# Kernel optimization log

Measured on AMD Instinct MI355X. Metric: run time of the kernel, lower is better.

The kernel has to match this reference:

```python
import jax, jax.numpy as jnp
import numpy as np

B, T, HID, H, DH, K = 2, 1024, 1024, 16, 64, 4
ROPE_BASE = 10000.0
EPS = 1e-6


def _causal_dwconv(x, w, b):
    # x: (B, T, C); w: (C, 1, K) depthwise; causal left-pad K-1, then SiLU
    xc = jnp.transpose(x, (0, 2, 1))  # (B, C, T)
    y = jax.lax.conv_general_dilated(
        xc, w, window_strides=(1,), padding=[(K - 1, 0)],
        dimension_numbers=('NCH', 'OIH', 'NCH'), feature_group_count=xc.shape[1])
    y = y + b[None, :, None]
    return jax.nn.silu(jnp.transpose(y, (0, 2, 1)))


def _rope(x, cos, sin):
    # x: (B, T, H, D); cos/sin: (T, D) with emb = cat(freqs, freqs)
    c = cos[None, :, None, :]
    s = sin[None, :, None, :]
    x1, x2 = x[..., ::2], x[..., 1::2]
    return jnp.concatenate(
        [x1 * c[..., ::2] - x2 * s[..., ::2],
         x1 * s[..., ::2] + x2 * c[..., ::2]], axis=-1)


def _delta_rule(q, k, v, alpha, beta, D_param):
    # q,k,v: (B,T,H,DH); alpha,beta: (B,T,H)
    # S_t = alpha_t * (I - beta_t k_t k_t^T) S_{t-1} + beta_t k_t v_t^T
    # o_t  = q_t^T S_t-1-style readout + D * (q.k) * v   (matches torch einsum 'bhd,bhde->bhe')
    qs = jnp.moveaxis(q, 1, 0).astype(jnp.float32)  # (T,B,H,DH)
    ks = jnp.moveaxis(k, 1, 0).astype(jnp.float32)
    vs = jnp.moveaxis(v, 1, 0).astype(jnp.float32)
    als = jnp.moveaxis(alpha, 1, 0).astype(jnp.float32)  # (T,B,H)
    bes = jnp.moveaxis(beta, 1, 0).astype(jnp.float32)

    def step(S, inp):
        qt, kt, vt, at, bt = inp
        ot = jnp.einsum('bhd,bhde->bhe', qt, S)
        ot = ot + D_param[None, :, None] * jnp.sum(qt * kt, -1, keepdims=True) * vt
        kS = jnp.einsum('bhd,bhde->bhe', kt, S)  # k^T S
        at_ = at[..., None, None]
        bt_ = bt[..., None, None]
        S_new = at_ * (S - bt_ * kt[..., :, None] * kS[..., None, :]) \
                + bt_ * kt[..., :, None] * vt[..., None, :]
        return S_new, ot

    S0 = jnp.zeros((q.shape[0], H, DH, DH), jnp.float32)
    _, outs = jax.lax.scan(step, S0, (qs, ks, vs, als, bes))
    return jnp.moveaxis(outs, 0, 1)  # (B,T,H,DH)


def _forward(x, Wq, Wk, Wv, Wg, Wo, bw, bb, gkw, gkb,
             qcw, qcb, kcw, kcb, vcw, vcb, A_log, D_param, dt_bias, onorm_w):
    Bb, Tt, _ = x.shape
    q = _causal_dwconv(x @ Wq, qcw, qcb).reshape(Bb, Tt, H, DH)
    k = _causal_dwconv(x @ Wk, kcw, kcb).reshape(Bb, Tt, H, DH)
    v = _causal_dwconv(x @ Wv, vcw, vcb).reshape(Bb, Tt, H, DH)

    # RoPE (computed on the fly, fp32)
    t = jnp.arange(Tt, dtype=jnp.float32)
    inv_freq = 1.0 / (ROPE_BASE ** (jnp.arange(0, DH, 2, dtype=jnp.float32) / DH))
    freqs = jnp.outer(t, inv_freq)
    emb = jnp.concatenate([freqs, freqs], -1)
    cos, sin = jnp.cos(emb), jnp.sin(emb)
    q = _rope(q, cos, sin)
    k = _rope(k, cos, sin)

    # L2-normalize q/k (delta-net stability, NOT softmax)
    q = q * jax.lax.rsqrt(jnp.sum(q * q, -1, keepdims=True) + EPS)
    k = k * jax.lax.rsqrt(jnp.sum(k * k, -1, keepdims=True) + EPS)

    beta = jax.nn.sigmoid(x @ bw + bb)  # (B,T,H) writing strength
    alpha = jnp.exp(-jnp.exp(A_log) * jax.nn.softplus(x @ gkw + gkb + dt_bias))  # (B,T,H) decay

    o = _delta_rule(q, k, v, alpha, beta, D_param)  # (B,T,H,DH)

    # gated RMSNorm output: g * silu(RMSNorm(o))
    g = (x @ Wg).reshape(Bb, Tt, H, DH)
    on = o * jax.lax.rsqrt(jnp.mean(o * o, -1, keepdims=True) + EPS) * onorm_w
    o = g * jax.nn.silu(on)
    return o.reshape(Bb, Tt, H * DH) @ Wo


def setup_inputs() -> dict:
    key = jax.random.key(0)
    ks = jax.random.split(key, 20)
    w = lambda i, shape, s=0.02: (jax.random.normal(ks[i], shape, jnp.float32) * s)
    return {
        'x': jax.random.normal(ks[0], (B, T, HID), jnp.float32),
        'Wq': w(1, (HID, H * DH)), 'Wk': w(2, (HID, H * DH)),
        'Wv': w(3, (HID, H * DH)), 'Wg': w(4, (HID, H * DH)),
        'Wo': w(5, (H * DH, HID)),
        'bw': w(6, (HID, H)), 'bb': jnp.zeros((H,), jnp.float32),
        'gkw': w(7, (HID, H)), 'gkb': jnp.zeros((H,), jnp.float32),
        'qcw': w(8, (H * DH, 1, K), 0.3), 'qcb': jnp.zeros((H * DH,), jnp.float32),
        'kcw': w(9, (H * DH, 1, K), 0.3), 'kcb': jnp.zeros((H * DH,), jnp.float32),
        'vcw': w(10, (H * DH, 1, K), 0.3), 'vcb': jnp.zeros((H * DH,), jnp.float32),
        'A_log': jnp.log(jax.random.uniform(ks[11], (H,), jnp.float32, 1.0, 16.0)),
        'D_param': jnp.ones((H,), jnp.float32),
        'dt_bias': jax.random.uniform(ks[12], (H,), jnp.float32, -0.01, 0.01),
        'onorm_w': jnp.ones((DH,), jnp.float32),
    }


def reference(x, Wq, Wk, Wv, Wg, Wo, bw, bb, gkw, gkb,
              qcw, qcb, kcw, kcb, vcw, vcb, A_log, D_param, dt_bias, onorm_w):
    return _forward(x, Wq, Wk, Wv, Wg, Wo, bw, bb, gkw, gkb,
                    qcw, qcb, kcw, kcb, vcw, vcb, A_log, D_param, dt_bias, onorm_w)
```

## Files before the change

kernel.cpp:

```cpp
#include <hip/hip_runtime.h>
#include <hip/hip_bf16.h>
#include <cstdint>

#define T_LEN 1024
#define HIDN  1024
#define NH    16
#define DHD   64

typedef __bf16 bf16x8 __attribute__((ext_vector_type(8)));
typedef float  f32x4  __attribute__((ext_vector_type(4)));

__device__ inline void split8(float4 x0, float4 x1, uint4& hi, uint4& lo) {
  union { __bf16 h[8]; uint4 u; } ph, pl;
  float v[8] = {x0.x, x0.y, x0.z, x0.w, x1.x, x1.y, x1.z, x1.w};
#pragma unroll
  for (int j = 0; j < 8; j++) {
    __bf16 h = (__bf16)v[j];
    ph.h[j] = h;
    pl.h[j] = (__bf16)(v[j] - (float)h);
  }
  hi = ph.u; lo = pl.u;
}

__global__ __launch_bounds__(256) void k_transp_split(
    const float* __restrict__ W0, const float* __restrict__ W1,
    const float* __restrict__ W2, const float* __restrict__ W3,
    const float* __restrict__ W4,
    __bf16* __restrict__ H0, __bf16* __restrict__ H1, __bf16* __restrict__ H2,
    __bf16* __restrict__ H3, __bf16* __restrict__ H4,
    __bf16* __restrict__ L0, __bf16* __restrict__ L1, __bf16* __restrict__ L2,
    __bf16* __restrict__ L3, __bf16* __restrict__ L4) {
  const float* W; __bf16* Th; __bf16* Tl;
  switch (blockIdx.z) {
    case 0: W = W0; Th = H0; Tl = L0; break;
    case 1: W = W1; Th = H1; Tl = L1; break;
    case 2: W = W2; Th = H2; Tl = L2; break;
    case 3: W = W3; Th = H3; Tl = L3; break;
    default: W = W4; Th = H4; Tl = L4; break;
  }
  __shared__ float tile[64][65];
  int tid = threadIdx.x;
  int r0 = tid >> 4;
  int c0 = (tid & 15) * 4;
  int kbase = blockIdx.y * 64, nbase = blockIdx.x * 64;
#pragma unroll
  for (int rr = 0; rr < 4; rr++) {
    int r = r0 + rr * 16;
    float4 v = *(const float4*)(W + (size_t)(kbase + r) * 1024 + nbase + c0);
    tile[r][c0 + 0] = v.x; tile[r][c0 + 1] = v.y;
    tile[r][c0 + 2] = v.z; tile[r][c0 + 3] = v.w;
  }
  __syncthreads();
#pragma unroll
  for (int rr = 0; rr < 4; rr++) {
    int n = r0 + rr * 16;
    union { __bf16 h[4]; unsigned long long u; } ph, pl;
#pragma unroll
    for (int j = 0; j < 4; j++) {
      float v = tile[c0 + j][n];
      __bf16 h = (__bf16)v;
      ph.h[j] = h;
      pl.h[j] = (__bf16)(v - (float)h);
    }
    *(unsigned long long*)(Th + (size_t)(nbase + n) * 1024 + kbase + c0) = ph.u;
    *(unsigned long long*)(Tl + (size_t)(nbase + n) * 1024 + kbase + c0) = pl.u;
  }
}

#define LDT 40
__global__ __launch_bounds__(256) void k_gemm3f(
    const float* __restrict__ Af,
    const __bf16* __restrict__ Bh0, const __bf16* __restrict__ Bh1,
    const __bf16* __restrict__ Bh2, const __bf16* __restrict__ Bh3,
    const __bf16* __restrict__ Bl0, const __bf16* __restrict__ Bl1,
    const __bf16* __restrict__ Bl2, const __bf16* __restrict__ Bl3,
    float* __restrict__ C0, float* __restrict__ C1,
    float* __restrict__ C2, float* __restrict__ C3,
    int Kdim, int Ncols) {
  const __bf16* Bh; const __bf16* Bl; float* C;
  switch (blockIdx.z) {
    case 0: Bh = Bh0; Bl = Bl0; C = C0; break;
    case 1: Bh = Bh1; Bl = Bl1; C = C1; break;
    case 2: Bh = Bh2; Bl = Bl2; C = C2; break;
    default: Bh = Bh3; Bl = Bl3; C = C3; break;
  }
  __shared__ __bf16 Ash[128 * LDT];
  __shared__ __bf16 Asl[128 * LDT];
  __shared__ __bf16 Bsh[128 * LDT];
  __shared__ __bf16 Bsl[128 * LDT];
  const int tid = threadIdx.x;
  const int lane = tid & 63;
  const int wave = tid >> 6;
  const int wr = wave >> 1, wc = wave & 1;
  const int rowA0 = blockIdx.y * 128;
  const int colB0 = blockIdx.x * 128;
  const int sseg = tid & 3;
  const int srow0 = tid >> 2;
  const int srow1 = srow0 + 64;

  f32x4 acc[4][4] = {};

  for (int k0 = 0; k0 < Kdim; k0 += 32) {
    size_t a0 = (size_t)(rowA0 + srow0) * Kdim + k0 + sseg * 8;
    size_t a1 = (size_t)(rowA0 + srow1) * Kdim + k0 + sseg * 8;
    size_t b0 = (size_t)(colB0 + srow0) * Kdim + k0 + sseg * 8;
    size_t b1 = (size_t)(colB0 + srow1) * Kdim + k0 + sseg * 8;
    float4 a00 = *(const float4*)(Af + a0);
    float4 a01 = *(const float4*)(Af + a0 + 4);
    float4 a10 = *(const float4*)(Af + a1);
    float4 a11 = *(const float4*)(Af + a1 + 4);
    uint4 rbh0 = *(const uint4*)(Bh + b0);
    uint4 rbh1 = *(const uint4*)(Bh + b1);
    uint4 rbl0 = *(const uint4*)(Bl + b0);
    uint4 rbl1 = *(const uint4*)(Bl + b1);
    uint4 rah0, ral0, rah1, ral1;
    split8(a00, a01, rah0, ral0);
    split8(a10, a11, rah1, ral1);
    __syncthreads();
    *(uint4*)&Ash[srow0 * LDT + sseg * 8] = rah0;
    *(uint4*)&Ash[srow1 * LDT + sseg * 8] = rah1;
    *(uint4*)&Asl[srow0 * LDT + sseg * 8] = ral0;
    *(uint4*)&Asl[srow1 * LDT + sseg * 8] = ral1;
    *(uint4*)&Bsh[srow0 * LDT + sseg * 8] = rbh0;
    *(uint4*)&Bsh[srow1 * LDT + sseg * 8] = rbh1;
    *(uint4*)&Bsl[srow0 * LDT + sseg * 8] = rbl0;
    *(uint4*)&Bsl[srow1 * LDT + sseg * 8] = rbl1;
    __syncthreads();
    bf16x8 afh[4], afl[4], bfh[4], bfl[4];
#pragma unroll
    for (int mi = 0; mi < 4; mi++) {
      int off = (wr * 64 + mi * 16 + (lane & 15)) * LDT + (lane >> 4) * 8;
      afh[mi] = *(const bf16x8*)&Ash[off];
      afl[mi] = *(const bf16x8*)&Asl[off];
    }
#pragma unroll
    for (int ni = 0; ni < 4; ni++) {
      int off = (wc * 64 + ni * 16 + (lane & 15)) * LDT + (lane >> 4) * 8;
      bfh[ni] = *(const bf16x8*)&Bsh[off];
      bfl[ni] = *(const bf16x8*)&Bsl[off];
    }
#pragma unroll
    for (int mi = 0; mi < 4; mi++)
#pragma unroll
      for (int ni = 0; ni < 4; ni++) {
        acc[mi][ni] = __builtin_amdgcn_mfma_f32_16x16x32_bf16(afh[mi], bfh[ni], acc[mi][ni], 0, 0, 0);
        acc[mi][ni] = __builtin_amdgcn_mfma_f32_16x16x32_bf16(afl[mi], bfh[ni], acc[mi][ni], 0, 0, 0);
        acc[mi][ni] = __builtin_amdgcn_mfma_f32_16x16x32_bf16(afh[mi], bfl[ni], acc[mi][ni], 0, 0, 0);
      }
  }
#pragma unroll
  for (int mi = 0; mi < 4; mi++)
#pragma unroll
    for (int ni = 0; ni < 4; ni++) {
      int col = colB0 + wc * 64 + ni * 16 + (lane & 15);
#pragma unroll
      for (int r = 0; r < 4; r++) {
        int row = rowA0 + wr * 64 + mi * 16 + (lane >> 4) * 4 + r;
        C[(size_t)row * Ncols + col] = acc[mi][ni][r];
      }
    }
}

__global__ __launch_bounds__(256) void k_gates(
    const float* __restrict__ x, const float* __restrict__ bw,
    const float* __restrict__ bb, const float* __restrict__ gkw,
    const float* __restrict__ gkb, const float* __restrict__ A_log,
    const float* __restrict__ dt_bias,
    float* __restrict__ alphaB, float* __restrict__ betaB) {
  const int bt = blockIdx.x;
  const int tid = threadIdx.x;
  const int h = tid & 15;
  const int chunk = tid >> 4;
  const float* xr = x + (size_t)bt * HIDN;
  float d1 = 0.f, d2 = 0.f;
#pragma unroll 8
  for (int j = 0; j < 64; j++) {
    int k = chunk * 64 + j;
    float xv = xr[k];
    d1 += xv * bw[k * 16 + h];
    d2 += xv * gkw[k * 16 + h];
  }
  __shared__ float p1[16][16], p2[16][16];
  p1[chunk][h] = d1; p2[chunk][h] = d2;
  __syncthreads();
  if (tid < 16) {
    float s1 = 0.f, s2 = 0.f;
#pragma unroll
    for (int c = 0; c < 16; c++) { s1 += p1[c][tid]; s2 += p2[c][tid]; }
    float beta = 1.f / (1.f + expf(-(s1 + bb[tid])));
    float z = s2 + gkb[tid] + dt_bias[tid];
    float sp = fmaxf(z, 0.f) + log1pf(expf(-fabsf(z)));
    float alpha = expf(-expf(A_log[tid]) * sp);
    alphaB[(size_t)bt * 16 + tid] = alpha;
    betaB[(size_t)bt * 16 + tid] = beta;
  }
}

__global__ __launch_bounds__(256) void k_cra(
    const float* __restrict__ qp, const float* __restrict__ kp,
    const float* __restrict__ vp,
    const float* __restrict__ qcw, const float* __restrict__ qcb,
    const float* __restrict__ kcw, const float* __restrict__ kcb,
    const float* __restrict__ vcw, const float* __restrict__ vcb,
    const float* __restrict__ alphaB, const float* __restrict__ betaB,
    const float* __restrict__ Dp,
    float* __restrict__ qr, float* __restrict__ kr, float* __restrict__ vr,
    float4* __restrict__ aux) {
  int widx = blockIdx.x * 4 + (threadIdx.x >> 6);
  int lane = threadIdx.x & 63;
  int h = widx & 15;
  int bt = widx >> 4;
  int t = bt & 1023, b = bt >> 10;
  int c = h * 64 + lane;
  size_t colbase = ((size_t)b * 1024) * 1024 + c;

  float4 wq = *(const float4*)(qcw + (size_t)c * 4);
  float4 wk = *(const float4*)(kcw + (size_t)c * 4);
  float4 wv = *(const float4*)(vcw + (size_t)c * 4);
  float aq = qcb[c], ak = kcb[c], av = vcb[c];
  {
    float x0 = qp[colbase + (size_t)t * 1024];
    float y0 = kp[colbase + (size_t)t * 1024];
    float z0 = vp[colbase + (size_t)t * 1024];
    aq += wq.w * x0; ak += wk.w * y0; av += wv.w * z0;
    if (t >= 1) {
      float x1 = qp[colbase + (size_t)(t - 1) * 1024];
      float y1 = kp[colbase + (size_t)(t - 1) * 1024];
      float z1 = vp[colbase + (size_t)(t - 1) * 1024];
      aq += wq.z * x1; ak += wk.z * y1; av += wv.z * z1;
    }
    if (t >= 2) {
      float x2 = qp[colbase + (size_t)(t - 2) * 1024];
      float y2 = kp[colbase + (size_t)(t - 2) * 1024];
      float z2v = vp[colbase + (size_t)(t - 2) * 1024];
      aq += wq.y * x2; ak += wk.y * y2; av += wv.y * z2v;
    }
    if (t >= 3) {
      float x3 = qp[colbase + (size_t)(t - 3) * 1024];
      float y3 = kp[colbase + (size_t)(t - 3) * 1024];
      float z3 = vp[colbase + (size_t)(t - 3) * 1024];
      aq += wq.x * x3; ak += wk.x * y3; av += wv.x * z3;
    }
  }
  float yq = aq / (1.f + expf(-aq));
  float yk = ak / (1.f + expf(-ak));
  float yv = av / (1.f + expf(-av));

  int i = lane & 31;
  float fr = expf(-(float)(2 * (i & 15)) * (9.210340371976184f / 32.f));
  float ang = (float)t * fr;
  float cv = cosf(ang), sv = sinf(ang);
  float q1 = __shfl(yq, 2 * i), q2 = __shfl(yq, 2 * i + 1);
  float k1 = __shfl(yk, 2 * i), k2 = __shfl(yk, 2 * i + 1);
  float qo = (lane < 32) ? (q1 * cv - q2 * sv) : (q1 * sv + q2 * cv);
  float ko = (lane < 32) ? (k1 * cv - k2 * sv) : (k1 * sv + k2 * cv);

  float qs = qo * qo, ks2 = ko * ko;
#pragma unroll
  for (int m = 1; m < 64; m <<= 1) { qs += __shfl_xor(qs, m); ks2 += __shfl_xor(ks2, m); }
  float qn = qo * rsqrtf(qs + 1e-6f);
  float kn = ko * rsqrtf(ks2 + 1e-6f);
  float dq = qn * kn;
#pragma unroll
  for (int m = 1; m < 64; m <<= 1) dq += __shfl_xor(dq, m);
  size_t obase = ((size_t)(b * 16 + h) * 1024 + t) * 64;
  qr[obase + lane] = qn;
  kr[obase + lane] = kn;
  vr[obase + lane] = yv;
  if (lane == 0) {
    float alpha = alphaB[(size_t)bt * 16 + h];
    float beta = betaB[(size_t)bt * 16 + h];
    aux[(size_t)(b * 16 + h) * 1024 + t] = make_float4(alpha, beta, alpha * beta, Dp[h] * dq);
  }
}

__global__ __launch_bounds__(128) void k_scanA(
    const float* __restrict__ qr, const float* __restrict__ kr,
    const float* __restrict__ vr, const float4* __restrict__ aux,
    float* __restrict__ O1, float* __restrict__ AcF,
    float* __restrict__ BcTF, float* __restrict__ QeffF,
    float* __restrict__ gcF) {
  const int bid = blockIdx.x;
  const int bh = bid >> 4, c = bid & 15;
  const int t0 = c * 64;
  const int tid = threadIdx.x;
  const int w = tid >> 6, lane = tid & 63;
  const float* qB = qr + (size_t)bh * 65536 + (size_t)t0 * 64;
  const float* kB = kr + (size_t)bh * 65536 + (size_t)t0 * 64;
  const float* vB = vr + (size_t)bh * 65536 + (size_t)t0 * 64;
  const float4* auxB = aux + (size_t)bh * T_LEN + t0;

  __shared__ __bf16 q_b[64 * 72];
  __shared__ __bf16 k_b[64 * 72];
  __shared__ __bf16 kT_b[64 * 72];
  __shared__ __bf16 C_b[64 * 72];
  __shared__ __bf16 U0T[64 * 72];
  __shared__ __bf16 WT[64 * 72];
  __shared__ float  vS[64 * 64];
  __shared__ float  MTf[64 * 68];
  __shared__ float  lgS[64], pvS[64], beS[64], awS[64], enS[64];

  if (w == 0) {
    float4 a4 = auxB[lane];
    float lg = logf(a4.x);
#pragma unroll
    for (int off = 1; off < 64; off <<= 1) {
      float tv = __shfl_up(lg, off);
      if (lane >= off) lg += tv;
    }
    float pv = __shfl_up(lg, 1);
    if (lane == 0) pv = 0.f;
    float lgTot = __shfl(lg, 63);
    lgS[lane] = lg; pvS[lane] = pv; beS[lane] = a4.y; awS[lane] = a4.w;
    enS[lane] = expf(lgTot - lg);
    if (lane == 0) gcF[bid] = expf(lgTot);
  }
#pragma unroll
  for (int p = 0; p < 4; p++) {
    int s = p * 128 + tid;
    int row = s >> 3, col8 = s & 7;
    const float* gq = qB + (size_t)row * 64 + col8 * 8;
    const float* gk = kB + (size_t)row * 64 + col8 * 8;
    const float* gv = vB + (size_t)row * 64 + col8 * 8;
    float4 q0 = *(const float4*)gq, q1 = *(const float4*)(gq + 4);
    float4 k0 = *(const float4*)gk, k1 = *(const float4*)(gk + 4);
    float4 v0 = *(const float4*)gv, v1 = *(const float4*)(gv + 4);
    union { __bf16 h[8]; uint4 u; } pq, pk;
    pq.h[0] = (__bf16)q0.x; pq.h[1] = (__bf16)q0.y; pq.h[2] = (__bf16)q0.z; pq.h[3] = (__bf16)q0.w;
    pq.h[4] = (__bf16)q1.x; pq.h[5] = (__bf16)q1.y; pq.h[6] = (__bf16)q1.z; pq.h[7] = (__bf16)q1.w;
    pk.h[0] = (__bf16)k0.x; pk.h[1] = (__bf16)k0.y; pk.h[2] = (__bf16)k0.z; pk.h[3] = (__bf16)k0.w;
    pk.h[4] = (__bf16)k1.x; pk.h[5] = (__bf16)k1.y; pk.h[6] = (__bf16)k1.z; pk.h[7] = (__bf16)k1.w;
    *(uint4*)&q_b[row * 72 + col8 * 8] = pq.u;
    *(uint4*)&k_b[row * 72 + col8 * 8] = pk.u;
    *(float4*)&vS[row * 64 + col8 * 8] = v0;
    *(float4*)&vS[row * 64 + col8 * 8 + 4] = v1;
  }
  __syncthreads();

#pragma unroll
  for (int mm = 0; mm < 2; mm++) {
    int mi = w * 2 + mm;
#pragma unroll
    for (int ni = 0; ni < 4; ni++) {
      f32x4 akk = {0.f, 0.f, 0.f, 0.f};
      f32x4 aqk = {0.f, 0.f, 0.f, 0.f};
#pragma unroll
      for (int ks = 0; ks < 2; ks++) {
        bf16x8 fa_k = *(const bf16x8*)&k_b[(mi * 16 + (lane & 15)) * 72 + ks * 32 + (lane >> 4) * 8];
        bf16x8 fa_q = *(const bf16x8*)&q_b[(mi * 16 + (lane & 15)) * 72 + ks * 32 + (lane >> 4) * 8];
        bf16x8 fb_k = *(const bf16x8*)&k_b[(ni * 16 + (lane & 15)) * 72 + ks * 32 + (lane >> 4) * 8];
        akk = __builtin_amdgcn_mfma_f32_16x16x32_bf16(fa_k, fb_k, akk, 0, 0, 0);
        aqk = __builtin_amdgcn_mfma_f32_16x16x32_bf16(fa_q, fb_k, aqk, 0, 0, 0);
      }
#pragma unroll
      for (int r = 0; r < 4; r++) {
        int row = mi * 16 + (lane >> 4) * 4 + r;
        int col = ni * 16 + (lane & 15);
        float mt = 0.f, cv = 0.f;
        if (row > col) {
          mt = beS[row] * expf(lgS[row] - lgS[col]) * akk[r];
          cv = expf(pvS[row] - lgS[col]) * aqk[r];
        }
        MTf[col * 68 + row] = mt;
        C_b[row * 72 + col] = (__bf16)cv;
      }
    }
  }
  __syncthreads();

  if (w == 1) {
#pragma unroll
    for (int t8 = 0; t8 < 8; t8++) {
      union { __bf16 h[8]; uint4 u; } pt;
#pragma unroll
      for (int q = 0; q < 8; q++) {
        int t = t8 * 8 + q;
        pt.h[q] = (__bf16)((float)k_b[t * 72 + lane] * enS[t]);
      }
      *(uint4*)&kT_b[lane * 72 + t8 * 8] = pt.u;
    }
  }

  {
    float u[64];
    if (w == 0) {
#pragma unroll
      for (int j = 0; j < 64; j++) u[j] = beS[j] * vS[j * 64 + lane];
    } else {
#pragma unroll
      for (int j = 0; j < 64; j++) u[j] = beS[j] * expf(lgS[j]) * (float)k_b[j * 72 + lane];
    }
    __bf16* dst = (w == 0) ? U0T : WT;
#pragma unroll
    for (int j = 0; j < 64; j++) {
      dst[lane * 72 + j] = (__bf16)u[j];
      float uj = u[j];
#pragma unroll
      for (int g = (j >> 4); g < 4; g++) {
#pragma unroll
        for (int q4 = 0; q4 < 4; q4++) {
          const float4 m4 = *(const float4*)&MTf[j * 68 + g * 16 + q4 * 4];
          u[g * 16 + q4 * 4 + 0] -= m4.x * uj;
          u[g * 16 + q4 * 4 + 1] -= m4.y * uj;
          u[g * 16 + q4 * 4 + 2] -= m4.z * uj;
          u[g * 16 + q4 * 4 + 3] -= m4.w * uj;
        }
      }
    }
  }
  __syncthreads();

  size_t cb = (size_t)bid * 4096;
  if (w == 0) {
#pragma unroll
    for (int mi = 0; mi < 4; mi++)
#pragma unroll
      for (int ni = 0; ni < 4; ni++) {
        f32x4 ab = {0.f, 0.f, 0.f, 0.f};
        f32x4 aa = {0.f, 0.f, 0.f, 0.f};
#pragma unroll
        for (int ks = 0; ks < 2; ks++) {
          int aoff = (mi * 16 + (lane & 15)) * 72 + ks * 32 + (lane >> 4) * 8;
          int boff = (ni * 16 + (lane & 15)) * 72 + ks * 32 + (lane >> 4) * 8;
          bf16x8 fu = *(const bf16x8*)&U0T[aoff];
          bf16x8 fkm = *(const bf16x8*)&kT_b[aoff];
          bf16x8 fkn = *(const bf16x8*)&kT_b[boff];
          bf16x8 fw = *(const bf16x8*)&WT[boff];
          ab = __builtin_amdgcn_mfma_f32_16x16x32_bf16(fu, fkn, ab, 0, 0, 0);
          aa = __builtin_amdgcn_mfma_f32_16x16x32_bf16(fkm, fw, aa, 0, 0, 0);
        }
#pragma unroll
        for (int r = 0; r < 4; r++) {
          int row = mi * 16 + (lane >> 4) * 4 + r;
          int col = ni * 16 + (lane & 15);
          BcTF[cb + row * 64 + col] = ab[r];
          AcF[cb + row * 64 + col] = aa[r];
        }
      }
  } else {
#pragma unroll
    for (int mi = 0; mi < 4; mi++)
#pragma unroll
      for (int ni = 0; ni < 4; ni++) {
        f32x4 ao = {0.f, 0.f, 0.f, 0.f};
        f32x4 ac = {0.f, 0.f, 0.f, 0.f};
#pragma unroll
        for (int ks = 0; ks < 2; ks++) {
          int aoff = (mi * 16 + (lane & 15)) * 72 + ks * 32 + (lane >> 4) * 8;
          int boff = (ni * 16 + (lane & 15)) * 72 + ks * 32 + (lane >> 4) * 8;
          bf16x8 fc = *(const bf16x8*)&C_b[aoff];
          bf16x8 fu = *(const bf16x8*)&U0T[boff];
          bf16x8 fw = *(const bf16x8*)&WT[boff];
          ao = __builtin_amdgcn_mfma_f32_16x16x32_bf16(fc, fu, ao, 0, 0, 0);
          ac = __builtin_amdgcn_mfma_f32_16x16x32_bf16(fc, fw, ac, 0, 0, 0);
        }
#pragma unroll
        for (int r = 0; r < 4; r++) {
          int t = mi * 16 + (lane >> 4) * 4 + r;
          int col = ni * 16 + (lane & 15);
          O1[(size_t)bh * 65536 + (size_t)(t0 + t) * 64 + col] =
              ao[r] + awS[t] * vS[t * 64 + col];
          QeffF[cb + t * 64 + col] = expf(pvS[t]) * (float)q_b[t * 72 + col] - ac[r];
        }
      }
  }
}

__global__ __launch_bounds__(256) void k_scanB(
    const float* __restrict__ AcF, const float* __restrict__ BcTF,
    const float* __restrict__ gcF, float* __restrict__ S0TF) {
  const int bh = blockIdx.x;
  const int tid = threadIdx.x;
  const int w = tid >> 6, lane = tid & 63;
  const int er = tid >> 2, seg = (tid & 3) * 16;
  __shared__ float STf[64 * 68];
  __shared__ __bf16 Sh[64 * 72], Sl[64 * 72], Ac_b[64 * 72];
#pragma unroll
  for (int i = 0; i < 4; i++)
    *(float4*)&STf[er * 68 + seg + i * 4] = make_float4(0.f, 0.f, 0.f, 0.f);
  __syncthreads();

  size_t cbase = (size_t)bh * 16 * 4096;
  float4 acR[4];
  float bctR[16];
#pragma unroll
  for (int i = 0; i < 4; i++)
    acR[i] = *(const float4*)&AcF[cbase + er * 64 + seg + i * 4];
#pragma unroll
  for (int r = 0; r < 4; r++)
#pragma unroll
    for (int ni = 0; ni < 4; ni++) {
      int e = w * 16 + (lane >> 4) * 4 + r;
      int d = ni * 16 + (lane & 15);
      bctR[r * 4 + ni] = BcTF[cbase + e * 64 + d];
    }

  for (int c = 0; c < 16; c++) {
    size_t cb = cbase + (size_t)c * 4096;
#pragma unroll
    for (int i = 0; i < 4; i++) {
      float4 s = *(const float4*)&STf[er * 68 + seg + i * 4];
      *(float4*)&S0TF[cb + er * 64 + seg + i * 4] = s;
      union { __bf16 h[4]; unsigned long long u; } ph, pl, pa;
      float sv[4] = {s.x, s.y, s.z, s.w};
      float av[4] = {acR[i].x, acR[i].y, acR[i].z, acR[i].w};
#pragma unroll
      for (int q = 0; q < 4; q++) {
        __bf16 hv = (__bf16)sv[q];
        ph.h[q] = hv;
        pl.h[q] = (__bf16)(sv[q] - (float)hv);
        pa.h[q] = (__bf16)av[q];
      }
      *(unsigned long long*)&Sh[er * 72 + seg + i * 4] = ph.u;
      *(unsigned long long*)&Sl[er * 72 + seg + i * 4] = pl.u;
      *(unsigned long long*)&Ac_b[er * 72 + seg + i * 4] = pa.u;
    }
    float gC = gcF[bh * 16 + c];
    __syncthreads();

    float4 acN[4];
    float bctN[16];
    if (c < 15) {
      size_t nb = cb + 4096;
#pragma unroll
      for (int i = 0; i < 4; i++)
        acN[i] = *(const float4*)&AcF[nb + er * 64 + seg + i * 4];
#pragma unroll
      for (int r = 0; r < 4; r++)
#pragma unroll
        for (int ni = 0; ni < 4; ni++) {
          int e = w * 16 + (lane >> 4) * 4 + r;
          int d = ni * 16 + (lane & 15);
          bctN[r * 4 + ni] = BcTF[nb + e * 64 + d];
        }
    } else {
#pragma unroll
      for (int i = 0; i < 4; i++) acN[i] = acR[i];
#pragma unroll
      for (int j = 0; j < 16; j++) bctN[j] = bctR[j];
    }

    f32x4 acc[4];
#pragma unroll
    for (int ni = 0; ni < 4; ni++) {
      acc[ni] = (f32x4){0.f, 0.f, 0.f, 0.f};
#pragma unroll
      for (int ks = 0; ks < 2; ks++) {
        int aoff = (w * 16 + (lane & 15)) * 72 + ks * 32 + (lane >> 4) * 8;
        int boff = (ni * 16 + (lane & 15)) * 72 + ks * 32 + (lane >> 4) * 8;
        bf16x8 ah = *(const bf16x8*)&Sh[aoff];
        bf16x8 al = *(const bf16x8*)&Sl[aoff];
        bf16x8 bb = *(const bf16x8*)&Ac_b[boff];
        acc[ni] = __builtin_amdgcn_mfma_f32_16x16x32_bf16(ah, bb, acc[ni], 0, 0, 0);
        acc[ni] = __builtin_amdgcn_mfma_f32_16x16x32_bf16(al, bb, acc[ni], 0, 0, 0);
      }
    }
#pragma unroll
    for (int ni = 0; ni < 4; ni++)
#pragma unroll
      for (int r = 0; r < 4; r++) {
        int e = w * 16 + (lane >> 4) * 4 + r;
        int d = ni * 16 + (lane & 15);
        STf[e * 68 + d] = gC * STf[e * 68 + d] - acc[ni][r] + bctR[r * 4 + ni];
      }
    __syncthreads();
#pragma unroll
    for (int i = 0; i < 4; i++) acR[i] = acN[i];
#pragma unroll
    for (int j = 0; j < 16; j++) bctR[j] = bctN[j];
  }
}

__global__ __launch_bounds__(256) void k_scanCn(
    const float* __restrict__ S0TF, const float* __restrict__ QeffF,
    const float* __restrict__ obuf, const float* __restrict__ g,
    const float* __restrict__ onw, float* __restrict__ robuf) {
  const int bid = blockIdx.x;
  const int bh = bid >> 4, c = bid & 15, t0c = c * 64;
  const int b = bh >> 4, h = bh & 15;
  const int tid = threadIdx.x;
  const int w = tid >> 6, lane = tid & 63;
  const int er = tid >> 2, seg = (tid & 3) * 16;
  size_t cb = (size_t)bid * 4096;
  __shared__ __bf16 Sh[64 * 72], Sl[64 * 72], Qb[64 * 72];
#pragma unroll
  for (int i = 0; i < 4; i++) {
    float4 s = *(const float4*)&S0TF[cb + er * 64 + seg + i * 4];
    union { __bf16 h[4]; unsigned long long u; } ph, pl;
    float sv[4] = {s.x, s.y, s.z, s.w};
#pragma unroll
    for (int q = 0; q < 4; q++) {
      __bf16 hv = (__bf16)sv[q];
      ph.h[q] = hv;
      pl.h[q] = (__bf16)(sv[q] - (float)hv);
    }
    *(unsigned long long*)&Sh[er * 72 + seg + i * 4] = ph.u;
    *(unsigned long long*)&Sl[er * 72 + seg + i * 4] = pl.u;
    float4 qq = *(const float4*)&QeffF[cb + er * 64 + seg + i * 4];
    union { __bf16 h[4]; unsigned long long u; } pq;
    pq.h[0] = (__bf16)qq.x; pq.h[1] = (__bf16)qq.y;
    pq.h[2] = (__bf16)qq.z; pq.h[3] = (__bf16)qq.w;
    *(unsigned long long*)&Qb[er * 72 + seg + i * 4] = pq.u;
  }
  __syncthreads();
  f32x4 acc[4];
#pragma unroll
  for (int ni = 0; ni < 4; ni++) {
    acc[ni] = (f32x4){0.f, 0.f, 0.f, 0.f};
#pragma unroll
    for (int ks = 0; ks < 2; ks++) {
      int aoff = (w * 16 + (lane & 15)) * 72 + ks * 32 + (lane >> 4) * 8;
      int boff = (ni * 16 + (lane & 15)) * 72 + ks * 32 + (lane >> 4) * 8;
      bf16x8 fq = *(const bf16x8*)&Qb[aoff];
      bf16x8 sh = *(const bf16x8*)&Sh[boff];
      bf16x8 sl = *(const bf16x8*)&Sl[boff];
      acc[ni] = __builtin_amdgcn_mfma_f32_16x16x32_bf16(fq, sh, acc[ni], 0, 0, 0);
      acc[ni] = __builtin_amdgcn_mfma_f32_16x16x32_bf16(fq, sl, acc[ni], 0, 0, 0);
    }
  }
  float onwv[4];
#pragma unroll
  for (int ni = 0; ni < 4; ni++) onwv[ni] = onw[ni * 16 + (lane & 15)];
#pragma unroll
  for (int r = 0; r < 4; r++) {
    int t = w * 16 + (lane >> 4) * 4 + r;
    float o[4];
#pragma unroll
    for (int ni = 0; ni < 4; ni++) {
      int e = ni * 16 + (lane & 15);
      o[ni] = obuf[(size_t)bh * 65536 + (size_t)(t0c + t) * 64 + e] + acc[ni][r];
    }
    float ss = o[0] * o[0] + o[1] * o[1] + o[2] * o[2] + o[3] * o[3];
    ss += __shfl_xor(ss, 1);
    ss += __shfl_xor(ss, 2);
    ss += __shfl_xor(ss, 4);
    ss += __shfl_xor(ss, 8);
    float rinv = rsqrtf(ss * (1.f / 64.f) + 1e-6f);
    size_t gbase = ((size_t)(b * 1024 + t0c + t)) * 1024 + h * 64;
#pragma unroll
    for (int ni = 0; ni < 4; ni++) {
      int e = ni * 16 + (lane & 15);
      float on = o[ni] * rinv * onwv[ni];
      float sil = on / (1.f + expf(-on));
      robuf[gbase + e] = g[gbase + e] * sil;
    }
  }
}

extern "C" void kernel_launch(void* const* d_in, const int* in_sizes, int n_in,
                              void* d_out, int out_size, void* d_ws, size_t ws_size,
                              hipStream_t stream) {
  (void)in_sizes; (void)n_in; (void)out_size; (void)ws_size;
  const float* x    = (const float*)d_in[0];
  const float* Wq   = (const float*)d_in[1];
  const float* Wk   = (const float*)d_in[2];
  const float* Wv   = (const float*)d_in[3];
  const float* Wg   = (const float*)d_in[4];
  const float* Wo   = (const float*)d_in[5];
  const float* bw   = (const float*)d_in[6];
  const float* bb   = (const float*)d_in[7];
  const float* gkw  = (const float*)d_in[8];
  const float* gkb  = (const float*)d_in[9];
  const float* qcw  = (const float*)d_in[10];
  const float* qcb  = (const float*)d_in[11];
  const float* kcw  = (const float*)d_in[12];
  const float* kcb  = (const float*)d_in[13];
  const float* vcw  = (const float*)d_in[14];
  const float* vcb  = (const float*)d_in[15];
  const float* A_log= (const float*)d_in[16];
  const float* Dp   = (const float*)d_in[17];
  const float* dtb  = (const float*)d_in[18];
  const float* onw  = (const float*)d_in[19];

  char* ws = (char*)d_ws;
  const size_t MB = 1024 * 1024;
  __bf16* Wq_h = (__bf16*)(ws + 8 * MB);
  __bf16* Wq_l = (__bf16*)(ws + 10 * MB);
  __bf16* Wk_h = (__bf16*)(ws + 12 * MB);
  __bf16* Wk_l = (__bf16*)(ws + 14 * MB);
  __bf16* Wv_h = (__bf16*)(ws + 16 * MB);
  __bf16* Wv_l = (__bf16*)(ws + 18 * MB);
  __bf16* Wg_h = (__bf16*)(ws + 20 * MB);
  __bf16* Wg_l = (__bf16*)(ws + 22 * MB);
  __bf16* Wo_h = (__bf16*)(ws + 24 * MB);
  __bf16* Wo_l = (__bf16*)(ws + 26 * MB);
  float* q_pre = (float*)(ws + 28 * MB);
  float* k_pre = (float*)(ws + 36 * MB);
  float* v_pre = (float*)(ws + 44 * MB);
  float* g_buf = (float*)(ws + 52 * MB);
  float* qrb   = (float*)(ws + 0);
  float* krb   = (float*)(ws + 8 * MB);
  float* vr    = (float*)(ws + 16 * MB);
  float* obuf  = v_pre;
  float* AcF   = (float*)(ws + 28 * MB);
  float* BcTF  = (float*)(ws + 36 * MB);
  float* S0TF  = (float*)(ws + 0);
  float* QeffF = (float*)(ws + 16 * MB);
  float* robuf = (float*)(ws + 8 * MB);
  float* alphaB = (float*)(ws + 60 * MB);
  float* betaB  = (float*)(ws + 60 * MB + 128 * 1024);
  float4* aux   = (float4*)(ws + 60 * MB + 256 * 1024);
  float* gcF    = (float*)(ws + 60 * MB + 768 * 1024);
  float* out    = (float*)d_out;

  k_transp_split<<<dim3(16, 16, 5), 256, 0, stream>>>(
      Wq, Wk, Wv, Wg, Wo,
      Wq_h, Wk_h, Wv_h, Wg_h, Wo_h,
      Wq_l, Wk_l, Wv_l, Wg_l, Wo_l);
  k_gates<<<2048, 256, 0, stream>>>(x, bw, bb, gkw, gkb, A_log, dtb, alphaB, betaB);
  k_gemm3f<<<dim3(8, 16, 4), 256, 0, stream>>>(
      x,
      Wq_h, Wk_h, Wv_h, Wg_h,
      Wq_l, Wk_l, Wv_l, Wg_l,
      q_pre, k_pre, v_pre, g_buf, 1024, 1024);
  k_cra<<<8192, 256, 0, stream>>>(q_pre, k_pre, v_pre,
                                  qcw, qcb, kcw, kcb, vcw, vcb,
                                  alphaB, betaB, Dp, qrb, krb, vr, aux);
  k_scanA<<<512, 128, 0, stream>>>(qrb, krb, vr, aux, obuf, AcF, BcTF, QeffF, gcF);
  k_scanB<<<32, 256, 0, stream>>>(AcF, BcTF, gcF, S0TF);
  k_scanCn<<<512, 256, 0, stream>>>(S0TF, QeffF, obuf, g_buf, onw, robuf);
  k_gemm3f<<<dim3(8, 16, 1), 256, 0, stream>>>(
      robuf,
      Wo_h, Wo_h, Wo_h, Wo_h,
      Wo_l, Wo_l, Wo_l, Wo_l,
      out, out, out, out, 1024, 1024);
}
```

Measured before the change: 335.7 us.

## Widen scanA to 256 threads and split scanB state rows across blocks

k_scanA now runs with four waves instead of two, so each wave owns one row tile in the intra-chunk MFMAs and half of the final output GEMMs, while two waves handle the triangular solve and a third builds the transposed K. k_scanB, the sequential inter-chunk state recurrence, is split over four blocks per head, each carrying a 16-row slice of the state. That raises the block count from 32 to 128 on a latency-bound serial loop. The cost is that each scanB block redundantly loads and converts the full Ac matrix every chunk, and in scanA two waves sit idle during the serial solve phase.

```diff
diff --git a/kernel.cpp b/kernel.cpp
--- a/kernel.cpp
+++ b/kernel.cpp
@@ -274,7 +274,7 @@
   }
 }
 
-__global__ __launch_bounds__(128) void k_scanA(
+__global__ __launch_bounds__(256) void k_scanA(
     const float* __restrict__ qr, const float* __restrict__ kr,
     const float* __restrict__ vr, const float4* __restrict__ aux,
     float* __restrict__ O1, float* __restrict__ AcF,
@@ -316,8 +316,8 @@
     if (lane == 0) gcF[bid] = expf(lgTot);
   }
 #pragma unroll
-  for (int p = 0; p < 4; p++) {
-    int s = p * 128 + tid;
+  for (int p = 0; p < 2; p++) {
+    int s = p * 256 + tid;
     int row = s >> 3, col8 = s & 7;
     const float* gq = qB + (size_t)row * 64 + col8 * 8;
     const float* gk = kB + (size_t)row * 64 + col8 * 8;
@@ -337,9 +337,8 @@
   }
   __syncthreads();
 
-#pragma unroll
-  for (int mm = 0; mm < 2; mm++) {
-    int mi = w * 2 + mm;
+  {
+    const int mi = w;
 #pragma unroll
     for (int ni = 0; ni < 4; ni++) {
       f32x4 akk = {0.f, 0.f, 0.f, 0.f};
@@ -368,7 +367,7 @@
   }
   __syncthreads();
 
-  if (w == 1) {
+  if (w == 2) {
 #pragma unroll
     for (int t8 = 0; t8 < 8; t8++) {
       union { __bf16 h[8]; uint4 u; } pt;
@@ -380,8 +379,7 @@
       *(uint4*)&kT_b[lane * 72 + t8 * 8] = pt.u;
     }
   }
-
-  {
+  if (w < 2) {
     float u[64];
     if (w == 0) {
 #pragma unroll
@@ -411,9 +409,11 @@
   __syncthreads();
 
   size_t cb = (size_t)bid * 4096;
-  if (w == 0) {
-#pragma unroll
-    for (int mi = 0; mi < 4; mi++)
+  const int mi0 = (w >> 1) * 2;
+  if ((w & 1) == 0) {
+#pragma unroll
+    for (int mm = 0; mm < 2; mm++) {
+      int mi = mi0 + mm;
 #pragma unroll
       for (int ni = 0; ni < 4; ni++) {
         f32x4 ab = {0.f, 0.f, 0.f, 0.f};
@@ -437,9 +437,11 @@
           AcF[cb + row * 64 + col] = aa[r];
         }
       }
+    }
   } else {
 #pragma unroll
-    for (int mi = 0; mi < 4; mi++)
+    for (int mm = 0; mm < 2; mm++) {
+      int mi = mi0 + mm;
 #pragma unroll
       for (int ni = 0; ni < 4; ni++) {
         f32x4 ao = {0.f, 0.f, 0.f, 0.f};
@@ -463,63 +465,63 @@
           QeffF[cb + t * 64 + col] = expf(pvS[t]) * (float)q_b[t * 72 + col] - ac[r];
         }
       }
+    }
   }
 }
 
 __global__ __launch_bounds__(256) void k_scanB(
     const float* __restrict__ AcF, const float* __restrict__ BcTF,
     const float* __restrict__ gcF, float* __restrict__ S0TF) {
-  const int bh = blockIdx.x;
+  const int bid = blockIdx.x;
+  const int bh = bid >> 2, eg = bid & 3;
+  const int e0 = eg * 16;
   const int tid = threadIdx.x;
   const int w = tid >> 6, lane = tid & 63;
   const int er = tid >> 2, seg = (tid & 3) * 16;
-  __shared__ float STf[64 * 68];
-  __shared__ __bf16 Sh[64 * 72], Sl[64 * 72], Ac_b[64 * 72];
-#pragma unroll
-  for (int i = 0; i < 4; i++)
-    *(float4*)&STf[er * 68 + seg + i * 4] = make_float4(0.f, 0.f, 0.f, 0.f);
+  const int er2 = tid >> 4, seg2 = (tid & 15) * 4;
+  __shared__ float STf[16 * 68];
+  __shared__ __bf16 Sh[16 * 72], Sl[16 * 72], Ac_b[64 * 72];
+  *(float4*)&STf[er2 * 68 + seg2] = make_float4(0.f, 0.f, 0.f, 0.f);
   __syncthreads();
 
   size_t cbase = (size_t)bh * 16 * 4096;
   float4 acR[4];
-  float bctR[16];
+  float bctR[4];
 #pragma unroll
   for (int i = 0; i < 4; i++)
     acR[i] = *(const float4*)&AcF[cbase + er * 64 + seg + i * 4];
 #pragma unroll
   for (int r = 0; r < 4; r++)
-#pragma unroll
-    for (int ni = 0; ni < 4; ni++) {
-      int e = w * 16 + (lane >> 4) * 4 + r;
-      int d = ni * 16 + (lane & 15);
-      bctR[r * 4 + ni] = BcTF[cbase + e * 64 + d];
-    }
+    bctR[r] = BcTF[cbase + (size_t)(e0 + (lane >> 4) * 4 + r) * 64 + w * 16 + (lane & 15)];
 
   for (int c = 0; c < 16; c++) {
     size_t cb = cbase + (size_t)c * 4096;
-#pragma unroll
-    for (int i = 0; i < 4; i++) {
-      float4 s = *(const float4*)&STf[er * 68 + seg + i * 4];
-      *(float4*)&S0TF[cb + er * 64 + seg + i * 4] = s;
-      union { __bf16 h[4]; unsigned long long u; } ph, pl, pa;
+    {
+      float4 s = *(const float4*)&STf[er2 * 68 + seg2];
+      *(float4*)&S0TF[cb + (size_t)(e0 + er2) * 64 + seg2] = s;
+      union { __bf16 h[4]; unsigned long long u; } ph, pl;
       float sv[4] = {s.x, s.y, s.z, s.w};
-      float av[4] = {acR[i].x, acR[i].y, acR[i].z, acR[i].w};
 #pragma unroll
       for (int q = 0; q < 4; q++) {
         __bf16 hv = (__bf16)sv[q];
         ph.h[q] = hv;
         pl.h[q] = (__bf16)(sv[q] - (float)hv);
-        pa.h[q] = (__bf16)av[q];
-      }
-      *(unsigned long long*)&Sh[er * 72 + seg + i * 4] = ph.u;
-      *(unsigned long long*)&Sl[er * 72 + seg + i * 4] = pl.u;
+      }
+      *(unsigned long long*)&Sh[er2 * 72 + seg2] = ph.u;
+      *(unsigned long long*)&Sl[er2 * 72 + seg2] = pl.u;
+    }
+#pragma unroll
+    for (int i = 0; i < 4; i++) {
+      union { __bf16 h[4]; unsigned long long u; } pa;
+      pa.h[0] = (__bf16)acR[i].x; pa.h[1] = (__bf16)acR[i].y;
+      pa.h[2] = (__bf16)acR[i].z; pa.h[3] = (__bf16)acR[i].w;
       *(unsigned long long*)&Ac_b[er * 72 + seg + i * 4] = pa.u;
     }
     float gC = gcF[bh * 16 + c];
     __syncthreads();
 
     float4 acN[4];
-    float bctN[16];
+    float bctN[4];
     if (c < 15) {
       size_t nb = cb + 4096;
 #pragma unroll
@@ -527,47 +529,36 @@
         acN[i] = *(const float4*)&AcF[nb + er * 64 + seg + i * 4];
 #pragma unroll
       for (int r = 0; r < 4; r++)
-#pragma unroll
-        for (int ni = 0; ni < 4; ni++) {
-          int e = w * 16 + (lane >> 4) * 4 + r;
-          int d = ni * 16 + (lane & 15);
-          bctN[r * 4 + ni] = BcTF[nb + e * 64 + d];
-        }
+        bctN[r] = BcTF[nb + (size_t)(e0 + (lane >> 4) * 4 + r) * 64 + w * 16 + (lane & 15)];
     } else {
 #pragma unroll
       for (int i = 0; i < 4; i++) acN[i] = acR[i];
 #pragma unroll
-      for (int j = 0; j < 16; j++) bctN[j] = bctR[j];
-    }
-
-    f32x4 acc[4];
-#pragma unroll
-    for (int ni = 0; ni < 4; ni++) {
-      acc[ni] = (f32x4){0.f, 0.f, 0.f, 0.f};
-#pragma unroll
-      for (int ks = 0; ks < 2; ks++) {
-        int aoff = (w * 16 + (lane & 15)) * 72 + ks * 32 + (lane >> 4) * 8;
-        int boff = (ni * 16 + (lane & 15)) * 72 + ks * 32 + (lane >> 4) * 8;
-        bf16x8 ah = *(const bf16x8*)&Sh[aoff];
-        bf16x8 al = *(const bf16x8*)&Sl[aoff];
-        bf16x8 bb = *(const bf16x8*)&Ac_b[boff];
-        acc[ni] = __builtin_amdgcn_mfma_f32_16x16x32_bf16(ah, bb, acc[ni], 0, 0, 0);
-        acc[ni] = __builtin_amdgcn_mfma_f32_16x16x32_bf16(al, bb, acc[ni], 0, 0, 0);
-      }
-    }
-#pragma unroll
-    for (int ni = 0; ni < 4; ni++)
-#pragma unroll
-      for (int r = 0; r < 4; r++) {
-        int e = w * 16 + (lane >> 4) * 4 + r;
-        int d = ni * 16 + (lane & 15);
-        STf[e * 68 + d] = gC * STf[e * 68 + d] - acc[ni][r] + bctR[r * 4 + ni];
-      }
+      for (int r = 0; r < 4; r++) bctN[r] = bctR[r];
+    }
+
+    f32x4 acc = {0.f, 0.f, 0.f, 0.f};
+#pragma unroll
+    for (int ks = 0; ks < 2; ks++) {
+      int aoff = (lane & 15) * 72 + ks * 32 + (lane >> 4) * 8;
+      int boff = (w * 16 + (lane & 15)) * 72 + ks * 32 + (lane >> 4) * 8;
+      bf16x8 ah = *(const bf16x8*)&Sh[aoff];
+      bf16x8 al = *(const bf16x8*)&Sl[aoff];
+      bf16x8 bb = *(const bf16x8*)&Ac_b[boff];
+      acc = __builtin_amdgcn_mfma_f32_16x16x32_bf16(ah, bb, acc, 0, 0, 0);
+      acc = __builtin_amdgcn_mfma_f32_16x16x32_bf16(al, bb, acc, 0, 0, 0);
+    }
+#pragma unroll
+    for (int r = 0; r < 4; r++) {
+      int e = (lane >> 4) * 4 + r;
+      int d = w * 16 + (lane & 15);
+      STf[e * 68 + d] = gC * STf[e * 68 + d] - acc[r] + bctR[r];
+    }
     __syncthreads();
 #pragma unroll
     for (int i = 0; i < 4; i++) acR[i] = acN[i];
 #pragma unroll
-    for (int j = 0; j < 16; j++) bctR[j] = bctN[j];
+    for (int r = 0; r < 4; r++) bctR[r] = bctN[r];
   }
 }
 
@@ -716,8 +707,8 @@
   k_cra<<<8192, 256, 0, stream>>>(q_pre, k_pre, v_pre,
                                   qcw, qcb, kcw, kcb, vcw, vcb,
                                   alphaB, betaB, Dp, qrb, krb, vr, aux);
-  k_scanA<<<512, 128, 0, stream>>>(qrb, krb, vr, aux, obuf, AcF, BcTF, QeffF, gcF);
-  k_scanB<<<32, 256, 0, stream>>>(AcF, BcTF, gcF, S0TF);
+  k_scanA<<<512, 256, 0, stream>>>(qrb, krb, vr, aux, obuf, AcF, BcTF, QeffF, gcF);
+  k_scanB<<<128, 256, 0, stream>>>(AcF, BcTF, gcF, S0TF);
   k_scanCn<<<512, 256, 0, stream>>>(S0TF, QeffF, obuf, g_buf, onw, robuf);
   k_gemm3f<<<dim3(8, 16, 1), 256, 0, stream>>>(
       robuf,
```

Measured after the change: 320.9 us. -4.4%, faster.
